# Optimization experiments

Hardware: AMD Instinct MI355X
Metric: run time of the kernel (lower is better)

The kernel has to match this reference:

```python
import jax, jax.numpy as jnp
import numpy as np

N = 50000   # total nodes
G = 500     # number of graphs
E = 800000  # edges
K = 5       # Chebyshev order


def cheb_conv(x, edge_index, W, b):
    """PyG ChebConv with sym normalization, lambda_max=2.0.
    L_hat = (2/lambda_max)(I - D^-1/2 A D^-1/2) - I = -D^-1/2 A D^-1/2.
    out = sum_k T_k(L_hat) x @ W[k] + b, with Chebyshev recurrence.
    W: [K, in, out].
    """
    row, col = edge_index[0], edge_index[1]
    deg = jax.ops.segment_sum(jnp.ones_like(row, dtype=x.dtype), row, num_segments=N)
    dinv = jnp.where(deg > 0, jax.lax.rsqrt(jnp.maximum(deg, 1e-12)), 0.0).astype(x.dtype)
    norm = -dinv[row] * dinv[col]  # [E]

    def Lx(h):  # sparse matvec: gather -> scale -> scatter-add
        return jax.ops.segment_sum(norm[:, None] * h[col], row, num_segments=N)

    Tx0 = x
    out = Tx0 @ W[0]
    Tx1 = Lx(Tx0)
    out = out + Tx1 @ W[1]
    for k in range(2, W.shape[0]):
        Tx2 = 2.0 * Lx(Tx1) - Tx0
        out = out + Tx2 @ W[k]
        Tx0, Tx1 = Tx1, Tx2
    return out + b


def setup_inputs() -> dict:
    key = jax.random.key(0)
    ks = jax.random.split(key, 12)
    F_in, C = 116, 2
    dims = [(F_in, 32), (32, 32), (32, 64), (64, 64), (64, 128)]
    inp = {}
    inp["x"] = jax.random.normal(ks[0], (N, F_in), dtype=jnp.float32)
    inp["edge_index"] = jax.random.randint(ks[1], (2, E), 0, N, dtype=jnp.int32)
    inp["batch"] = jnp.sort(jax.random.randint(ks[2], (N,), 0, G, dtype=jnp.int32))
    for i, (di, do) in enumerate(dims):
        scale = 1.0 / np.sqrt(di * K)
        inp[f"W{i+1}"] = jax.random.normal(ks[3 + i], (K, di, do), dtype=jnp.float32) * scale
        inp[f"b{i+1}"] = jnp.zeros((do,), dtype=jnp.float32)
    inp["lin_w"] = jax.random.normal(ks[10], (128, C), dtype=jnp.float32) * (1.0 / np.sqrt(128))
    inp["lin_b"] = jnp.zeros((C,), dtype=jnp.float32)
    return inp


def reference(x, edge_index, batch, W1, b1, W2, b2, W3, b3, W4, b4, W5, b5, lin_w, lin_b):
    h = jax.nn.relu(cheb_conv(x, edge_index, W1, b1))
    h = jax.nn.relu(cheb_conv(h, edge_index, W2, b2))
    # dropout is identity in eval mode
    h = jax.nn.relu(cheb_conv(h, edge_index, W3, b3))
    h = jax.nn.relu(cheb_conv(h, edge_index, W4, b4))
    h = jax.nn.relu(cheb_conv(h, edge_index, W5, b5))
    # global mean pool over graph ids
    cnt = jax.ops.segment_sum(jnp.ones((N,), h.dtype), batch, num_segments=G)
    summ = jax.ops.segment_sum(h, batch, num_segments=G)  # [G, 128]
    pooled = summ / jnp.maximum(cnt, 1.0)[:, None]
    logits = pooled @ lin_w + lin_b  # [G, C]
    return jax.nn.log_softmax(logits, axis=1)
```

## Files before the change

### kernel.cpp

```cpp
#include <hip/hip_runtime.h>

#define N_NODES 50000
#define N_GRAPHS 500
#define N_EDGES 800000

static inline int cdiv(int a, int b) { return (a + b - 1) / b; }

typedef _Float16 half8v __attribute__((ext_vector_type(8)));
typedef _Float16 half4v __attribute__((ext_vector_type(4)));
typedef __attribute__((ext_vector_type(4))) float f32x4;

__device__ __forceinline__ _Float16 f2h(float f) { return (_Float16)f; }


__global__ void count_kernel(const int* __restrict__ row, int* __restrict__ cnt, int e) {
    int t = blockIdx.x * blockDim.x + threadIdx.x;
    if (t < e) atomicAdd(&cnt[row[t]], 1);
}

__global__ void block_scan_kernel(const int* __restrict__ cnt, int* __restrict__ rp,
                                  int* __restrict__ bsum, int n) {
    __shared__ int buf[2][256];
    int t = threadIdx.x;
    int idx = blockIdx.x * 256 + t;
    int v = (idx < n) ? cnt[idx] : 0;
    buf[0][t] = v;
    __syncthreads();
    int s = 0;
#pragma unroll
    for (int off = 1; off < 256; off <<= 1) {
        int x = buf[s][t];
        if (t >= off) x += buf[s][t - off];
        buf[s ^ 1][t] = x;
        s ^= 1;
        __syncthreads();
    }
    if (idx < n) rp[idx] = buf[s][t] - v;
    if (t == 255) bsum[blockIdx.x] = buf[s][255];
}

__global__ void scan_bsum_kernel(int* __restrict__ bsum, int nb) {
    __shared__ int buf[2][256];
    int t = threadIdx.x;
    int v = (t < nb) ? bsum[t] : 0;
    buf[0][t] = v;
    __syncthreads();
    int s = 0;
#pragma unroll
    for (int off = 1; off < 256; off <<= 1) {
        int x = buf[s][t];
        if (t >= off) x += buf[s][t - off];
        buf[s ^ 1][t] = x;
        s ^= 1;
        __syncthreads();
    }
    if (t < nb) bsum[t] = buf[s][t] - v;
}

__global__ void add_off_kernel(int* __restrict__ rp, const int* __restrict__ bsum, int n) {
    int idx = blockIdx.x * 256 + threadIdx.x;
    if (idx < n) rp[idx] += bsum[idx >> 8];
    if (idx == 0) rp[n] = N_EDGES;
}

__global__ void dinv_cursor_kernel(const int* __restrict__ cnt, const int* __restrict__ rp,
                                   float* __restrict__ dinv, int* __restrict__ cursor, int n) {
    int t = blockIdx.x * blockDim.x + threadIdx.x;
    if (t < n) {
        int c = cnt[t];
        dinv[t] = (c > 0) ? rsqrtf((float)c) : 0.0f;
        cursor[t] = rp[t];
    }
}

__global__ void fill_kernel(const int* __restrict__ row, const int* __restrict__ col,
                            const float* __restrict__ dinv, int* __restrict__ cursor,
                            unsigned* __restrict__ ew, int e) {
    int t = blockIdx.x * blockDim.x + threadIdx.x;
    if (t < e) {
        int r = row[t], c = col[t];
        int slot = atomicAdd(&cursor[r], 1);
        float w = -dinv[r] * dinv[c];
        unsigned short wb = __builtin_bit_cast(unsigned short, (_Float16)w);
        ew[slot] = ((unsigned)c << 16) | (unsigned)wb;
    }
}


__global__ void conv_x_kernel(const float* __restrict__ x, _Float16* __restrict__ xh) {
    int t = blockIdx.x * blockDim.x + threadIdx.x;
    if (t >= N_NODES * 128) return;
    int r = t >> 7, c = t & 127;
    xh[t] = (c < 116) ? f2h(x[(size_t)r * 116 + c]) : (_Float16)0.f;
}

__global__ void conv_wt1_kernel(const float* __restrict__ W, _Float16* __restrict__ wt) {
    int t = blockIdx.x * blockDim.x + threadIdx.x;
    if (t >= 160 * 128) return;
    int c = t >> 7, k = t & 127;
    wt[t] = (k < 116) ? f2h(W[(c >> 5) * (116 * 32) + k * 32 + (c & 31)]) : (_Float16)0.f;
}

template <int FOUT, int KB>
__global__ void conv_wt_kernel(const float* __restrict__ W, _Float16* __restrict__ wt) {
    int t = blockIdx.x * blockDim.x + threadIdx.x;
    if (t >= FOUT * KB) return;
    int c = t / KB, k = t % KB;
    wt[t] = f2h(W[(size_t)k * FOUT + c]);
}


template <int F, bool HAS_A, bool HAS_B, bool RELU>
__global__ __launch_bounds__(256) void spmm_fused(
    const int* __restrict__ rp, const unsigned* __restrict__ ew,
    const _Float16* __restrict__ src, int ld_s, float alpha,
    const _Float16* __restrict__ A, int ldA, float cA,
    const _Float16* __restrict__ B, int ldB, float cB,
    const float* __restrict__ bias, _Float16* __restrict__ outh, int ldO) {
    constexpr int TPN = F / 4;
    int t = blockIdx.x * blockDim.x + threadIdx.x;
    if (t >= N_NODES * TPN) return;
    int node = t / TPN;
    int f = (t % TPN) * 4;
    const _Float16* sf = src + f;
    int e0 = rp[node], e1 = rp[node + 1];
    float ax = 0.f, ay = 0.f, az = 0.f, aw = 0.f;
    int j = e0;
    for (; j + 3 < e1; j += 4) {
        unsigned ea = ew[j], eb = ew[j + 1], ec = ew[j + 2], ed = ew[j + 3];
        float w0 = (float)__builtin_bit_cast(_Float16, (unsigned short)ea);
        float w1 = (float)__builtin_bit_cast(_Float16, (unsigned short)eb);
        float w2 = (float)__builtin_bit_cast(_Float16, (unsigned short)ec);
        float w3 = (float)__builtin_bit_cast(_Float16, (unsigned short)ed);
        half4v v0 = *(const half4v*)(sf + (size_t)(ea >> 16) * ld_s);
        half4v v1 = *(const half4v*)(sf + (size_t)(eb >> 16) * ld_s);
        half4v v2 = *(const half4v*)(sf + (size_t)(ec >> 16) * ld_s);
        half4v v3 = *(const half4v*)(sf + (size_t)(ed >> 16) * ld_s);
        ax += w0 * (float)v0.x + w1 * (float)v1.x + w2 * (float)v2.x + w3 * (float)v3.x;
        ay += w0 * (float)v0.y + w1 * (float)v1.y + w2 * (float)v2.y + w3 * (float)v3.y;
        az += w0 * (float)v0.z + w1 * (float)v1.z + w2 * (float)v2.z + w3 * (float)v3.z;
        aw += w0 * (float)v0.w + w1 * (float)v1.w + w2 * (float)v2.w + w3 * (float)v3.w;
    }
    for (; j < e1; ++j) {
        unsigned ea = ew[j];
        float w0 = (float)__builtin_bit_cast(_Float16, (unsigned short)ea);
        half4v v0 = *(const half4v*)(sf + (size_t)(ea >> 16) * ld_s);
        ax += w0 * (float)v0.x;
        ay += w0 * (float)v0.y;
        az += w0 * (float)v0.z;
        aw += w0 * (float)v0.w;
    }
    float rx = alpha * ax, ry = alpha * ay, rz = alpha * az, rw = alpha * aw;
    if (HAS_A) {
        half4v a4 = *(const half4v*)(A + (size_t)node * ldA + f);
        rx += cA * (float)a4.x; ry += cA * (float)a4.y;
        rz += cA * (float)a4.z; rw += cA * (float)a4.w;
    }
    if (HAS_B) {
        half4v b4 = *(const half4v*)(B + (size_t)node * ldB + f);
        rx += cB * (float)b4.x; ry += cB * (float)b4.y;
        rz += cB * (float)b4.z; rw += cB * (float)b4.w;
    }
    if (RELU) {
        float4 bb = *(const float4*)(bias + f);
        rx = fmaxf(rx + bb.x, 0.f); ry = fmaxf(ry + bb.y, 0.f);
        rz = fmaxf(rz + bb.z, 0.f); rw = fmaxf(rw + bb.w, 0.f);
    }
    half4v h4;
    h4.x = f2h(rx); h4.y = f2h(ry); h4.z = f2h(rz); h4.w = f2h(rw);
    *(half4v*)(outh + (size_t)node * ldO + f) = h4;
}


template <int KB, int F0, int FOUT, bool DUAL, bool RELU>
__global__ __launch_bounds__(256) void mm_mfma(const _Float16* __restrict__ A0h,
                                               const _Float16* __restrict__ A1h,
                                               const _Float16* __restrict__ Wt,
                                               const float* __restrict__ bias,
                                               _Float16* __restrict__ outh) {
    constexpr int NT = FOUT / 16;
    constexpr int LD1 = (KB - F0) > 0 ? (KB - F0) : 1;
    int tid = threadIdx.x;
    int l = tid & 63;
    int w = tid >> 6;
    int row0 = blockIdx.x * 64 + w * 16;
    int r15 = l & 15;
    int kg = l >> 4;
    int rr = row0 + r15;
    if (rr > N_NODES - 1) rr = N_NODES - 1;

    f32x4 acc[NT];
#pragma unroll
    for (int ct = 0; ct < NT; ++ct) acc[ct] = (f32x4){0.f, 0.f, 0.f, 0.f};

#pragma unroll
    for (int k0 = 0; k0 < KB; k0 += 32) {
        int kl = k0 + kg * 8;
        const _Float16* ap;
        if (!DUAL || k0 < F0)
            ap = A0h + (size_t)rr * F0 + kl;
        else
            ap = A1h + (size_t)rr * LD1 + (kl - F0);
        half8v af = *(const half8v*)ap;
#pragma unroll
        for (int ct = 0; ct < NT; ++ct) {
            const _Float16* bp = Wt + (size_t)(ct * 16 + r15) * KB + kl;
            half8v bf = *(const half8v*)bp;
            acc[ct] = __builtin_amdgcn_mfma_f32_16x16x32_f16(af, bf, acc[ct], 0, 0, 0);
        }
    }

    int orow = row0 + kg * 4;
#pragma unroll
    for (int ct = 0; ct < NT; ++ct) {
        int col = ct * 16 + r15;
        float bv = RELU ? bias[col] : 0.f;
#pragma unroll
        for (int i = 0; i < 4; ++i) {
            int rw = orow + i;
            if (rw < N_NODES) {
                float v = acc[ct][i];
                if (RELU) v = fmaxf(v + bv, 0.f);
                outh[(size_t)rw * FOUT + col] = f2h(v);
            }
        }
    }
}


__global__ void pool_head_kernel(const _Float16* __restrict__ h, const int* __restrict__ batch,
                                 const float* __restrict__ lw, const float* __restrict__ lb,
                                 float* __restrict__ out) {
    int g = blockIdx.x;
    int f = threadIdx.x;
    int s, e;
    {
        int lo = 0, hi = N_NODES;
        while (lo < hi) { int mid = (lo + hi) >> 1; if (batch[mid] < g) lo = mid + 1; else hi = mid; }
        s = lo;
        hi = N_NODES;
        while (lo < hi) { int mid = (lo + hi) >> 1; if (batch[mid] < g + 1) lo = mid + 1; else hi = mid; }
        e = lo;
    }
    float sum = 0.0f;
    for (int i = s; i < e; ++i) sum += (float)h[(size_t)i * 128 + f];
    float cnt = (float)(e - s);
    float pooled = sum / fmaxf(cnt, 1.0f);

    __shared__ float l0[128], l1[128];
    l0[f] = pooled * lw[f * 2 + 0];
    l1[f] = pooled * lw[f * 2 + 1];
    __syncthreads();
    for (int sdt = 64; sdt > 0; sdt >>= 1) {
        if (f < sdt) { l0[f] += l0[f + sdt]; l1[f] += l1[f + sdt]; }
        __syncthreads();
    }
    if (f == 0) {
        float a = l0[0] + lb[0], b = l1[0] + lb[1];
        float m = fmaxf(a, b);
        float lse = m + logf(expf(a - m) + expf(b - m));
        out[g * 2 + 0] = a - lse;
        out[g * 2 + 1] = b - lse;
    }
}


template <int F, int FOUT>
static void run_layer_fwd(const _Float16* hh, _Float16* Zh, _Float16* houth,
                          const _Float16* Wt, const float* b, const int* rp,
                          const unsigned* ew, hipStream_t s) {
    constexpr int TPN = F / 4;
    int sp_grid = cdiv(N_NODES * TPN, 256);
    int mm_grid = cdiv(N_NODES, 64);
    const _Float16* nh_ = nullptr;
    spmm_fused<F, false, false, false><<<sp_grid, 256, 0, s>>>(
        rp, ew, hh, F, 1.f, nh_, 0, 0.f, nh_, 0, 0.f, nullptr, Zh + 0 * F, 4 * F);
    spmm_fused<F, true, false, false><<<sp_grid, 256, 0, s>>>(
        rp, ew, Zh + 0 * F, 4 * F, 2.f, hh, F, -1.f, nh_, 0, 0.f, nullptr, Zh + 1 * F, 4 * F);
    spmm_fused<F, true, false, false><<<sp_grid, 256, 0, s>>>(
        rp, ew, Zh + 1 * F, 4 * F, 2.f, Zh + 0 * F, 4 * F, -1.f, nh_, 0, 0.f, nullptr, Zh + 2 * F, 4 * F);
    spmm_fused<F, true, false, false><<<sp_grid, 256, 0, s>>>(
        rp, ew, Zh + 2 * F, 4 * F, 2.f, Zh + 1 * F, 4 * F, -1.f, nh_, 0, 0.f, nullptr, Zh + 3 * F, 4 * F);
    mm_mfma<5 * F, F, FOUT, true, true><<<mm_grid, 256, 0, s>>>(hh, Zh, Wt, b, houth);
}

extern "C" void kernel_launch(void* const* d_in, const int* in_sizes, int n_in,
                              void* d_out, int out_size, void* d_ws, size_t ws_size,
                              hipStream_t stream) {
    const float* x = (const float*)d_in[0];
    const int* ei = (const int*)d_in[1];
    const int* batch = (const int*)d_in[2];
    const float* W1 = (const float*)d_in[3];
    const float* b1 = (const float*)d_in[4];
    const float* W2 = (const float*)d_in[5];
    const float* b2 = (const float*)d_in[6];
    const float* W3 = (const float*)d_in[7];
    const float* b3 = (const float*)d_in[8];
    const float* W4 = (const float*)d_in[9];
    const float* b4 = (const float*)d_in[10];
    const float* W5 = (const float*)d_in[11];
    const float* b5 = (const float*)d_in[12];
    const float* lin_w = (const float*)d_in[13];
    const float* lin_b = (const float*)d_in[14];
    const int* row = ei;
    const int* col = ei + N_EDGES;
    float* out = (float*)d_out;

    char* p = (char*)d_ws;
    auto alloc = [&](size_t bytes) {
        char* r = p;
        p += (bytes + 255) & ~(size_t)255;
        return r;
    };
    int* cnt = (int*)alloc((size_t)N_NODES * 4);
    int* rp = (int*)alloc((size_t)(N_NODES + 1) * 4);
    int* cursor = (int*)alloc((size_t)N_NODES * 4);
    int* bsum = (int*)alloc(256 * 4);
    float* dinv = (float*)alloc((size_t)N_NODES * 4);
    unsigned* ew = (unsigned*)alloc((size_t)N_EDGES * 4);
    _Float16* Zh = (_Float16*)alloc((size_t)N_NODES * 256 * 2);
    _Float16* hAh = (_Float16*)alloc((size_t)N_NODES * 128 * 2);
    _Float16* hBh = (_Float16*)alloc((size_t)N_NODES * 128 * 2);
    _Float16* wt1 = (_Float16*)alloc((size_t)160 * 128 * 2);
    _Float16* wt2 = (_Float16*)alloc((size_t)32 * 160 * 2);
    _Float16* wt3 = (_Float16*)alloc((size_t)64 * 160 * 2);
    _Float16* wt4 = (_Float16*)alloc((size_t)64 * 320 * 2);
    _Float16* wt5 = (_Float16*)alloc((size_t)128 * 320 * 2);

    const int NB = cdiv(N_NODES, 256);
    hipMemsetAsync(cnt, 0, (size_t)N_NODES * 4, stream);
    count_kernel<<<cdiv(N_EDGES, 256), 256, 0, stream>>>(row, cnt, N_EDGES);
    block_scan_kernel<<<NB, 256, 0, stream>>>(cnt, rp, bsum, N_NODES);
    scan_bsum_kernel<<<1, 256, 0, stream>>>(bsum, NB);
    add_off_kernel<<<NB, 256, 0, stream>>>(rp, bsum, N_NODES);
    dinv_cursor_kernel<<<cdiv(N_NODES, 256), 256, 0, stream>>>(cnt, rp, dinv, cursor, N_NODES);
    fill_kernel<<<cdiv(N_EDGES, 256), 256, 0, stream>>>(row, col, dinv, cursor, ew, N_EDGES);

    conv_x_kernel<<<cdiv(N_NODES * 128, 256), 256, 0, stream>>>(x, hAh);
    conv_wt1_kernel<<<cdiv(160 * 128, 256), 256, 0, stream>>>(W1, wt1);
    conv_wt_kernel<32, 160><<<cdiv(32 * 160, 256), 256, 0, stream>>>(W2, wt2);
    conv_wt_kernel<64, 160><<<cdiv(64 * 160, 256), 256, 0, stream>>>(W3, wt3);
    conv_wt_kernel<64, 320><<<cdiv(64 * 320, 256), 256, 0, stream>>>(W4, wt4);
    conv_wt_kernel<128, 320><<<cdiv(128 * 320, 256), 256, 0, stream>>>(W5, wt5);

    _Float16* Uh = Zh;
    const _Float16* nh_ = nullptr;
    mm_mfma<128, 128, 160, false, false><<<cdiv(N_NODES, 64), 256, 0, stream>>>(
        hAh, nh_, wt1, nullptr, Uh);
    _Float16* B3h = hBh;
    _Float16* B2h = hBh + (size_t)N_NODES * 32;
    _Float16* B1h = hBh + (size_t)N_NODES * 64;
    _Float16* h1h = hAh;
    int g32 = cdiv(N_NODES * 8, 256);
    spmm_fused<32, true, false, false><<<g32, 256, 0, stream>>>(
        rp, ew, Uh + 128, 160, 2.f, Uh + 96, 160, 1.f, nh_, 0, 0.f, nullptr, B3h, 32);
    spmm_fused<32, true, true, false><<<g32, 256, 0, stream>>>(
        rp, ew, B3h, 32, 2.f, Uh + 64, 160, 1.f, Uh + 128, 160, -1.f, nullptr, B2h, 32);
    spmm_fused<32, true, true, false><<<g32, 256, 0, stream>>>(
        rp, ew, B2h, 32, 2.f, Uh + 32, 160, 1.f, B3h, 32, -1.f, nullptr, B1h, 32);
    spmm_fused<32, true, true, true><<<g32, 256, 0, stream>>>(
        rp, ew, B1h, 32, 1.f, Uh + 0, 160, 1.f, B2h, 32, -1.f, b1, h1h, 32);

    run_layer_fwd<32, 32>(h1h, Zh, hBh, wt2, b2, rp, ew, stream);
    run_layer_fwd<32, 64>(hBh, Zh, hAh, wt3, b3, rp, ew, stream);
    run_layer_fwd<64, 64>(hAh, Zh, hBh, wt4, b4, rp, ew, stream);
    run_layer_fwd<64, 128>(hBh, Zh, hAh, wt5, b5, rp, ew, stream);

    pool_head_kernel<<<N_GRAPHS, 128, 0, stream>>>(hAh, batch, lin_w, lin_b, out);
}
```

Measured before the change: 682.3 us.

## Stage weight tiles in shared memory for MFMA GEMM and unroll SpMM gather by 8

The MFMA GEMM kernel now copies chunks of the transposed weight matrix into padded LDS once per block and reads B fragments from LDS instead of re-reading them from global memory in every wave. The SpMM kernel gains an 8-wide unrolled edge loop that issues all eight index loads and gathers before accumulating, to expose more memory-level parallelism. The LDS staging adds barriers and shared-memory use per block, and it assumes KB is a multiple of the 160-wide chunk, which can lower occupancy. The deeper unroll raises register pressure.

```diff
diff --git a/kernel.cpp b/kernel.cpp
--- a/kernel.cpp
+++ b/kernel.cpp
@@ -126,20 +126,37 @@
     int e0 = rp[node], e1 = rp[node + 1];
     float ax = 0.f, ay = 0.f, az = 0.f, aw = 0.f;
     int j = e0;
+    for (; j + 7 < e1; j += 8) {
+        unsigned e_[8];
+#pragma unroll
+        for (int u = 0; u < 8; ++u) e_[u] = ew[j + u];
+        half4v v_[8];
+#pragma unroll
+        for (int u = 0; u < 8; ++u) v_[u] = *(const half4v*)(sf + (size_t)(e_[u] >> 16) * ld_s);
+#pragma unroll
+        for (int u = 0; u < 8; ++u) {
+            float w = (float)__builtin_bit_cast(_Float16, (unsigned short)e_[u]);
+            ax += w * (float)v_[u].x;
+            ay += w * (float)v_[u].y;
+            az += w * (float)v_[u].z;
+            aw += w * (float)v_[u].w;
+        }
+    }
     for (; j + 3 < e1; j += 4) {
-        unsigned ea = ew[j], eb = ew[j + 1], ec = ew[j + 2], ed = ew[j + 3];
-        float w0 = (float)__builtin_bit_cast(_Float16, (unsigned short)ea);
-        float w1 = (float)__builtin_bit_cast(_Float16, (unsigned short)eb);
-        float w2 = (float)__builtin_bit_cast(_Float16, (unsigned short)ec);
-        float w3 = (float)__builtin_bit_cast(_Float16, (unsigned short)ed);
-        half4v v0 = *(const half4v*)(sf + (size_t)(ea >> 16) * ld_s);
-        half4v v1 = *(const half4v*)(sf + (size_t)(eb >> 16) * ld_s);
-        half4v v2 = *(const half4v*)(sf + (size_t)(ec >> 16) * ld_s);
-        half4v v3 = *(const half4v*)(sf + (size_t)(ed >> 16) * ld_s);
-        ax += w0 * (float)v0.x + w1 * (float)v1.x + w2 * (float)v2.x + w3 * (float)v3.x;
-        ay += w0 * (float)v0.y + w1 * (float)v1.y + w2 * (float)v2.y + w3 * (float)v3.y;
-        az += w0 * (float)v0.z + w1 * (float)v1.z + w2 * (float)v2.z + w3 * (float)v3.z;
-        aw += w0 * (float)v0.w + w1 * (float)v1.w + w2 * (float)v2.w + w3 * (float)v3.w;
+        unsigned e_[4];
+#pragma unroll
+        for (int u = 0; u < 4; ++u) e_[u] = ew[j + u];
+        half4v v_[4];
+#pragma unroll
+        for (int u = 0; u < 4; ++u) v_[u] = *(const half4v*)(sf + (size_t)(e_[u] >> 16) * ld_s);
+#pragma unroll
+        for (int u = 0; u < 4; ++u) {
+            float w = (float)__builtin_bit_cast(_Float16, (unsigned short)e_[u]);
+            ax += w * (float)v_[u].x;
+            ay += w * (float)v_[u].y;
+            az += w * (float)v_[u].z;
+            aw += w * (float)v_[u].w;
+        }
     }
     for (; j < e1; ++j) {
         unsigned ea = ew[j];
@@ -180,6 +197,11 @@
                                                _Float16* __restrict__ outh) {
     constexpr int NT = FOUT / 16;
     constexpr int LD1 = (KB - F0) > 0 ? (KB - F0) : 1;
+    constexpr int KC = (KB > 160) ? 160 : KB;
+    constexpr int NCH = KB / KC;
+    constexpr int LDW = KC + 8;
+    __shared__ _Float16 lw[FOUT][LDW];
+
     int tid = threadIdx.x;
     int l = tid & 63;
     int w = tid >> 6;
@@ -194,20 +216,31 @@
     for (int ct = 0; ct < NT; ++ct) acc[ct] = (f32x4){0.f, 0.f, 0.f, 0.f};
 
 #pragma unroll
-    for (int k0 = 0; k0 < KB; k0 += 32) {
-        int kl = k0 + kg * 8;
-        const _Float16* ap;
-        if (!DUAL || k0 < F0)
-            ap = A0h + (size_t)rr * F0 + kl;
-        else
-            ap = A1h + (size_t)rr * LD1 + (kl - F0);
-        half8v af = *(const half8v*)ap;
-#pragma unroll
-        for (int ct = 0; ct < NT; ++ct) {
-            const _Float16* bp = Wt + (size_t)(ct * 16 + r15) * KB + kl;
-            half8v bf = *(const half8v*)bp;
-            acc[ct] = __builtin_amdgcn_mfma_f32_16x16x32_f16(af, bf, acc[ct], 0, 0, 0);
+    for (int ch = 0; ch < NCH; ++ch) {
+        constexpr int C8 = KC / 8;
+        int c0 = ch * KC;
+        for (int idx = tid; idx < FOUT * C8; idx += 256) {
+            int r = idx / C8, c8 = idx - r * C8;
+            *(half8v*)&lw[r][c8 * 8] = *(const half8v*)(Wt + (size_t)r * KB + c0 + c8 * 8);
         }
+        __syncthreads();
+#pragma unroll
+        for (int k0 = 0; k0 < KC; k0 += 32) {
+            int gc = c0 + k0;
+            int kl = gc + kg * 8;
+            const _Float16* ap;
+            if (!DUAL || gc < F0)
+                ap = A0h + (size_t)rr * F0 + kl;
+            else
+                ap = A1h + (size_t)rr * LD1 + (kl - F0);
+            half8v af = *(const half8v*)ap;
+#pragma unroll
+            for (int ct = 0; ct < NT; ++ct) {
+                half8v bf = *(const half8v*)&lw[ct * 16 + r15][k0 + kg * 8];
+                acc[ct] = __builtin_amdgcn_mfma_f32_16x16x32_f16(af, bf, acc[ct], 0, 0, 0);
+            }
+        }
+        __syncthreads();
     }
 
     int orow = row0 + kg * 4;
```

Result: faster. 621.0 us (-9.0%).
